# Kernel optimization log

Measured on AMD Instinct MI355X. Metric: run time of the kernel, lower is better.

The kernel has to match this reference:

```python
import jax, jax.numpy as jnp
import numpy as np

# dims
B, S = 1, 32768          # batch, grid seqlen (32^3 latent grid)
NQ, NE = 32768, 262144   # mesh query nodes, grid->query edges
IN, EMB, HID, BOT, PREDH, OUT, NDIM = 192, 192, 192, 192, 192, 4, 3
MAX_WAVELENGTH = 10000.0


def sincos_embed(coords, dim, ndim):
    # ContinuousSincosEmbed: dim % ndim == 0 and (dim//ndim) even here -> no padding
    eff = dim // ndim                                     # 64 dims per coordinate
    omega = 1.0 / MAX_WAVELENGTH ** (jnp.arange(0, eff, 2, dtype=jnp.float32) / eff)  # [eff//2]
    out = coords[..., None] * omega                       # [N, ndim, eff//2]
    emb = jnp.concatenate([jnp.sin(out), jnp.cos(out)], axis=-1)  # [N, ndim, eff]
    return emb.reshape(coords.shape[0], ndim * eff)       # [N, dim]


def _linear_params(key, fan_in, fan_out):
    k1, k2 = jax.random.split(key)
    lim = 1.0 / np.sqrt(fan_in)
    w = jax.random.uniform(k1, (fan_in, fan_out), jnp.float32, -lim, lim)
    b = jax.random.uniform(k2, (fan_out,), jnp.float32, -lim, lim)
    return w, b


def setup_inputs() -> dict:
    key = jax.random.key(0)
    ks = jax.random.split(key, 10)
    x = jax.random.normal(ks[0], (B, S, IN), jnp.float32)
    query_pos = jax.random.uniform(ks[1], (NQ, NDIM), jnp.float32) * 100.0
    # edges sorted by query index (required by the CSR segment reduce in the original)
    qidx = jnp.sort(jax.random.randint(ks[2], (NE,), 0, NQ))
    gidx = jax.random.randint(ks[3], (NE,), 0, B * S)
    grid_to_query_edges = jnp.stack([qidx, gidx], axis=1).astype(jnp.int64)
    proj_w, proj_b = _linear_params(ks[4], IN, EMB)
    msg0_w, msg0_b = _linear_params(ks[5], 2 * EMB, 2 * HID)
    msg1_w, msg1_b = _linear_params(ks[6], 2 * HID, 2 * HID)
    msg2_w, msg2_b = _linear_params(ks[7], 2 * HID, BOT)
    pred0_w, pred0_b = _linear_params(ks[8], BOT, PREDH)
    pred1_w, pred1_b = _linear_params(ks[9], PREDH, OUT)
    return dict(x=x, query_pos=query_pos, grid_to_query_edges=grid_to_query_edges,
                proj_w=proj_w, proj_b=proj_b,
                msg0_w=msg0_w, msg0_b=msg0_b, msg1_w=msg1_w, msg1_b=msg1_b,
                msg2_w=msg2_w, msg2_b=msg2_b,
                pred0_w=pred0_w, pred0_b=pred0_b, pred1_w=pred1_w, pred1_b=pred1_b)


def reference(x, query_pos, grid_to_query_edges,
              proj_w, proj_b, msg0_w, msg0_b, msg1_w, msg1_b, msg2_w, msg2_b,
              pred0_w, pred0_b, pred1_w, pred1_b):
    gelu = lambda t: jax.nn.gelu(t, approximate=False)  # torch nn.GELU default (erf)
    # flatten grid tokens and project
    xf = x.reshape(-1, x.shape[-1]) @ proj_w + proj_b          # [B*S, EMB]
    qe = sincos_embed(query_pos, EMB, NDIM)                    # [NQ, EMB]
    qidx = grid_to_query_edges[:, 0]
    gidx = grid_to_query_edges[:, 1]
    # gather + concat per edge
    h = jnp.concatenate([xf[gidx], qe[qidx]], axis=1)          # [NE, 2*EMB]
    # message MLP
    h = gelu(h @ msg0_w + msg0_b)
    h = gelu(h @ msg1_w + msg1_b)
    h = h @ msg2_w + msg2_b                                    # [NE, BOT]
    # segment mean to query nodes (empty segments -> 0, matching segment_csr mean)
    nq = query_pos.shape[0]
    seg_sum = jax.ops.segment_sum(h, qidx, num_segments=nq)    # [NQ, BOT]
    cnt = jax.ops.segment_sum(jnp.ones((qidx.shape[0], 1), h.dtype), qidx, num_segments=nq)
    m = seg_sum / jnp.maximum(cnt, 1.0)
    # prediction head
    out = gelu(m @ pred0_w + pred0_b) @ pred1_w + pred1_b      # [NQ, OUT]
    return out
```

## Files before the change

kernel.cpp:

```cpp
#include <hip/hip_runtime.h>
#include <math.h>

#define N_Q    32768
#define N_E    262144

typedef _Float16 half8 __attribute__((ext_vector_type(8)));
typedef _Float16 half4v __attribute__((ext_vector_type(4)));
typedef float f32x4 __attribute__((ext_vector_type(4)));

__device__ __forceinline__ float gelu_f(float x) {
    float ax = fabsf(x);
    float t = __builtin_amdgcn_rcpf(fmaf(0.33269070724668f, ax, 1.0f));
    float poly = t * fmaf(t, fmaf(t, 0.7478556f, -0.0958798f), 0.3480242f);
    float e = exp2f(-0.72134752044448f * ax * ax);
    float u = fmaf(-poly, e, 1.0f);
    return 0.5f * fmaf(ax, u, x);
}

__global__ __launch_bounds__(256) void prep_kernel(
    const float* __restrict__ proj_w, const float* __restrict__ proj_b,
    const float* __restrict__ msg0_w, const float* __restrict__ msg0_b,
    float* __restrict__ Wc, float* __restrict__ bc)
{
    int gid = blockIdx.x * 256 + threadIdx.x;
    if (gid < 73728) {
        int j = gid / 384, n = gid - j * 384;
        float a = 0.0f;
        for (int k = 0; k < 192; ++k)
            a = fmaf(proj_w[j * 192 + k], msg0_w[k * 384 + n], a);
        Wc[gid] = a;
    } else if (gid < 73728 + 384) {
        int n = gid - 73728;
        float a = msg0_b[n];
        for (int k = 0; k < 192; ++k)
            a = fmaf(proj_b[k], msg0_w[k * 384 + n], a);
        bc[n] = a;
    }
}

__device__ __forceinline__ void pack_one(const float* __restrict__ W,
                                         _Float16* __restrict__ Wp,
                                         int K, int N, int blk0, int tid) {
    int u = blk0 * 256 + tid;
    if (u * 8 >= K * N) return;
    int l = u & 63, blk = u >> 6;
    int nks = K >> 5;
    int ntile = blk / nks, ks = blk - ntile * nks;
    int n = ntile * 16 + (l & 15);
    int k0 = ks * 32 + (l >> 4) * 8;
    half8 v;
    #pragma unroll
    for (int j = 0; j < 8; ++j) v[j] = (_Float16)W[(size_t)(k0 + j) * N + n];
    *(half8*)(Wp + (size_t)u * 8) = v;
}

__global__ __launch_bounds__(256) void pack_all_kernel(
    const float* __restrict__ Wc,  _Float16* __restrict__ WpC,
    const float* __restrict__ m0,  _Float16* __restrict__ WpQ,
    const float* __restrict__ m1,  _Float16* __restrict__ Wp1,
    const float* __restrict__ m2,  _Float16* __restrict__ Wp2,
    const float* __restrict__ hw,  _Float16* __restrict__ WpH) {
    int b = blockIdx.x, t = threadIdx.x;
    if      (b < 36)  pack_one(Wc,          WpC, 192, 384, b,       t);
    else if (b < 72)  pack_one(m0 + 73728,  WpQ, 192, 384, b - 36,  t);
    else if (b < 144) pack_one(m1,          Wp1, 384, 384, b - 72,  t);
    else if (b < 180) pack_one(m2,          Wp2, 384, 192, b - 144, t);
    else              pack_one(hw,          WpH, 192, 192, b - 180, t);
}

#define PK 200

__global__ __launch_bounds__(256, 2) void pg_kernel(
    const float* __restrict__ x, const _Float16* __restrict__ WpC,
    const float* __restrict__ bc, _Float16* __restrict__ pg)
{
    __shared__ _Float16 hA[64 * PK];
    const int t = threadIdx.x;
    const int r0 = blockIdx.x * 64;
    const int lane = t & 63;
    const int w = t >> 6;
    const int ln = lane & 15, lq = lane >> 4;

    #pragma unroll
    for (int i = 0; i < 12; ++i) {
        int idx = t + 256 * i;
        int r = idx / 48, c4 = idx - r * 48;
        float4 v = ((const float4*)(x + (size_t)(r0 + r) * 192))[c4];
        half4v hv; hv[0] = (_Float16)v.x; hv[1] = (_Float16)v.y;
        hv[2] = (_Float16)v.z; hv[3] = (_Float16)v.w;
        *(half4v*)(hA + r * PK + c4 * 4) = hv;
    }
    __syncthreads();

    f32x4 acc[4][6];
    #pragma unroll
    for (int nt = 0; nt < 6; ++nt) {
        f32x4 bv = *(const f32x4*)(bc + w * 96 + nt * 16 + lq * 4);
        #pragma unroll
        for (int mt = 0; mt < 4; ++mt) acc[mt][nt] = bv;
    }
    #pragma unroll 2
    for (int ks = 0; ks < 6; ++ks) {
        half8 a[4], bf[6];
        #pragma unroll
        for (int mt = 0; mt < 4; ++mt)
            a[mt] = *(const half8*)(hA + (mt * 16 + ln) * PK + ks * 32 + lq * 8);
        #pragma unroll
        for (int nt = 0; nt < 6; ++nt)
            bf[nt] = *(const half8*)(WpC + (size_t)(((w * 6 + nt) * 6 + ks) * 512 + lane * 8));
        #pragma unroll
        for (int nt = 0; nt < 6; ++nt)
            #pragma unroll
            for (int mt = 0; mt < 4; ++mt)
                acc[mt][nt] = __builtin_amdgcn_mfma_f32_16x16x32_f16(bf[nt], a[mt], acc[mt][nt], 0, 0, 0);
    }
    #pragma unroll
    for (int mt = 0; mt < 4; ++mt)
        #pragma unroll
        for (int nt = 0; nt < 6; ++nt) {
            half4v hv;
            #pragma unroll
            for (int r = 0; r < 4; ++r) hv[r] = (_Float16)acc[mt][nt][r];
            *(half4v*)(pg + (size_t)(r0 + mt * 16 + ln) * 384 + w * 96 + nt * 16 + lq * 4) = hv;
        }
}

__global__ __launch_bounds__(256, 2) void pq_kernel(
    const float* __restrict__ qpos, const _Float16* __restrict__ WpQ,
    _Float16* __restrict__ pq)
{
    __shared__ _Float16 hA[64 * PK];
    const int t = threadIdx.x;
    const int r0 = blockIdx.x * 64;
    const int lane = t & 63;
    const int w = t >> 6;
    const int ln = lane & 15, lq = lane >> 4;

    #pragma unroll
    for (int it = 0; it < 24; ++it) {
        int g2 = t + 256 * it;
        int r = g2 / 96, rem = g2 - r * 96;
        int d = rem >> 5, i = rem & 31;
        float omega = exp2f(-(float)i * 0.41524101186092029f);
        float arg = qpos[(size_t)(r0 + r) * 3 + d] * omega;
        float rev = arg * 0.15915494309189535f;
        rev = rev - floorf(rev);
        hA[r * PK + d * 64 + i]      = (_Float16)__builtin_amdgcn_sinf(rev);
        hA[r * PK + d * 64 + 32 + i] = (_Float16)__builtin_amdgcn_cosf(rev);
    }
    __syncthreads();

    f32x4 acc[4][6];
    #pragma unroll
    for (int nt = 0; nt < 6; ++nt)
        #pragma unroll
        for (int mt = 0; mt < 4; ++mt) acc[mt][nt] = (f32x4){0.f, 0.f, 0.f, 0.f};
    #pragma unroll 2
    for (int ks = 0; ks < 6; ++ks) {
        half8 a[4], bf[6];
        #pragma unroll
        for (int mt = 0; mt < 4; ++mt)
            a[mt] = *(const half8*)(hA + (mt * 16 + ln) * PK + ks * 32 + lq * 8);
        #pragma unroll
        for (int nt = 0; nt < 6; ++nt)
            bf[nt] = *(const half8*)(WpQ + (size_t)(((w * 6 + nt) * 6 + ks) * 512 + lane * 8));
        #pragma unroll
        for (int nt = 0; nt < 6; ++nt)
            #pragma unroll
            for (int mt = 0; mt < 4; ++mt)
                acc[mt][nt] = __builtin_amdgcn_mfma_f32_16x16x32_f16(bf[nt], a[mt], acc[mt][nt], 0, 0, 0);
    }
    #pragma unroll
    for (int mt = 0; mt < 4; ++mt)
        #pragma unroll
        for (int nt = 0; nt < 6; ++nt) {
            half4v hv;
            #pragma unroll
            for (int r = 0; r < 4; ++r) hv[r] = (_Float16)acc[mt][nt][r];
            *(half4v*)(pq + (size_t)(r0 + mt * 16 + ln) * 384 + w * 96 + nt * 16 + lq * 4) = hv;
        }
}

#define PADK 392
#define H2S  196

__global__ __launch_bounds__(512, 6) void edge_mlp_kernel(
    const _Float16* __restrict__ pg, const _Float16* __restrict__ pq,
    const int* __restrict__ edges,
    const _Float16* __restrict__ Wp1, const float* __restrict__ b1,
    const _Float16* __restrict__ Wp2, const float* __restrict__ b2,
    float* __restrict__ seg, float* __restrict__ cnt)
{
    __shared__ _Float16 hA[64 * PADK];
    __shared__ int qi[64];
    float* h2 = (float*)hA;

    const int t = threadIdx.x;
    const int e0 = blockIdx.x * 64;
    const int lane = t & 63;
    const int w = t >> 6;
    const int ln = lane & 15;
    const int lq = lane >> 4;

    if (t < 64) qi[t] = edges[2 * (e0 + t)];

    {
        const int m = t >> 3;
        const int cl = t & 7;
        int2 eg = ((const int2*)edges)[e0 + m];
        const half8* gsrc = (const half8*)(pg + (size_t)eg.y * 384) + cl;
        const half8* qsrc = (const half8*)(pq + (size_t)eg.x * 384) + cl;
        half8* dst = (half8*)(hA + m * PADK + cl * 8);
        #pragma unroll
        for (int i = 0; i < 6; ++i) {
            half8 va = gsrc[i * 8];
            half8 vb = qsrc[i * 8];
            half8 o;
            #pragma unroll
            for (int j = 0; j < 8; ++j)
                o[j] = (_Float16)gelu_f((float)va[j] + (float)vb[j]);
            dst[i * 8] = o;
        }
    }
    __syncthreads();

    {
        f32x4 acc[4][3];
        #pragma unroll
        for (int nt = 0; nt < 3; ++nt) {
            f32x4 bv = *(const f32x4*)(b1 + w * 48 + nt * 16 + lq * 4);
            #pragma unroll
            for (int mt = 0; mt < 4; ++mt) acc[mt][nt] = bv;
        }
        #pragma unroll 2
        for (int ks = 0; ks < 12; ++ks) {
            half8 a[4], bf[3];
            #pragma unroll
            for (int mt = 0; mt < 4; ++mt)
                a[mt] = *(const half8*)(hA + (mt * 16 + ln) * PADK + ks * 32 + lq * 8);
            #pragma unroll
            for (int nt = 0; nt < 3; ++nt)
                bf[nt] = *(const half8*)(Wp1 + (size_t)(((w * 3 + nt) * 12 + ks) * 512 + lane * 8));
            #pragma unroll
            for (int nt = 0; nt < 3; ++nt)
                #pragma unroll
                for (int mt = 0; mt < 4; ++mt)
                    acc[mt][nt] = __builtin_amdgcn_mfma_f32_16x16x32_f16(bf[nt], a[mt], acc[mt][nt], 0, 0, 0);
        }
        __syncthreads();
        #pragma unroll
        for (int mt = 0; mt < 4; ++mt)
            #pragma unroll
            for (int nt = 0; nt < 3; ++nt) {
                half4v hv;
                #pragma unroll
                for (int r = 0; r < 4; ++r) hv[r] = (_Float16)gelu_f(acc[mt][nt][r]);
                *(half4v*)(hA + (mt * 16 + ln) * PADK + w * 48 + nt * 16 + lq * 4) = hv;
            }
        __syncthreads();
    }

    {
        const int n0 = (w & 3) * 48;
        const int mh = (w >> 2) * 2;
        f32x4 acc[2][3];
        #pragma unroll
        for (int nt = 0; nt < 3; ++nt) {
            f32x4 bv = *(const f32x4*)(b2 + n0 + nt * 16 + lq * 4);
            #pragma unroll
            for (int mt = 0; mt < 2; ++mt) acc[mt][nt] = bv;
        }
        #pragma unroll 2
        for (int ks = 0; ks < 12; ++ks) {
            half8 a[2], bf[3];
            #pragma unroll
            for (int mt = 0; mt < 2; ++mt)
                a[mt] = *(const half8*)(hA + ((mh + mt) * 16 + ln) * PADK + ks * 32 + lq * 8);
            #pragma unroll
            for (int nt = 0; nt < 3; ++nt)
                bf[nt] = *(const half8*)(Wp2 + (size_t)((((w & 3) * 3 + nt) * 12 + ks) * 512 + lane * 8));
            #pragma unroll
            for (int nt = 0; nt < 3; ++nt)
                #pragma unroll
                for (int mt = 0; mt < 2; ++mt)
                    acc[mt][nt] = __builtin_amdgcn_mfma_f32_16x16x32_f16(bf[nt], a[mt], acc[mt][nt], 0, 0, 0);
        }
        __syncthreads();
        #pragma unroll
        for (int mt = 0; mt < 2; ++mt)
            #pragma unroll
            for (int nt = 0; nt < 3; ++nt)
                *(f32x4*)(h2 + ((mh + mt) * 16 + ln) * H2S + n0 + nt * 16 + lq * 4) = acc[mt][nt];
        __syncthreads();
    }

    if (t < 384) {
        int half_ = t >= 192;
        int col = t - half_ * 192;
        int mlo = half_ * 32, mhi = mlo + 32;
        float a = 0.0f;
        for (int m = mlo; m < mhi; ++m) {
            a += h2[m * H2S + col];
            if (m == mhi - 1 || qi[m + 1] != qi[m]) {
                atomicAdd(&seg[(size_t)qi[m] * 192 + col], a);
                a = 0.0f;
            }
        }
    } else if (t < 386) {
        int half_ = t - 384;
        int mlo = half_ * 32, mhi = mlo + 32;
        float run = 1.0f;
        for (int m = mlo + 1; m < mhi; ++m) {
            if (qi[m] != qi[m - 1]) { atomicAdd(&cnt[qi[m - 1]], run); run = 1.0f; }
            else run += 1.0f;
        }
        atomicAdd(&cnt[qi[mhi - 1]], run);
    }
}

#define PSK 196

__global__ __launch_bounds__(256, 2) void head_kernel(
    const float* __restrict__ seg, const float* __restrict__ cnt,
    const _Float16* __restrict__ Wp0, const float* __restrict__ b0,
    const float* __restrict__ w1, const float* __restrict__ b1,
    float* __restrict__ out)
{
    __shared__ _Float16 hA[64 * PK];
    __shared__ float ps[64 * PSK];
    __shared__ float w1s[192 * 4];
    __shared__ float invc[64];
    const int t = threadIdx.x;
    const int r0 = blockIdx.x * 64;
    const int lane = t & 63;
    const int w = t >> 6;
    const int ln = lane & 15, lq = lane >> 4;

    if (t < 64) invc[t] = 1.0f / fmaxf(cnt[r0 + t], 1.0f);
    if (t < 192) ((float4*)w1s)[t] = ((const float4*)w1)[t];
    __syncthreads();

    #pragma unroll
    for (int i = 0; i < 12; ++i) {
        int idx = t + 256 * i;
        int r = idx / 48, c4 = idx - r * 48;
        float inv = invc[r];
        float4 v = ((const float4*)(seg + (size_t)(r0 + r) * 192))[c4];
        half4v hv; hv[0] = (_Float16)(v.x * inv); hv[1] = (_Float16)(v.y * inv);
        hv[2] = (_Float16)(v.z * inv); hv[3] = (_Float16)(v.w * inv);
        *(half4v*)(hA + r * PK + c4 * 4) = hv;
    }
    __syncthreads();

    f32x4 acc[4][3];
    #pragma unroll
    for (int nt = 0; nt < 3; ++nt) {
        f32x4 bv = *(const f32x4*)(b0 + w * 48 + nt * 16 + lq * 4);
        #pragma unroll
        for (int mt = 0; mt < 4; ++mt) acc[mt][nt] = bv;
    }
    #pragma unroll 2
    for (int ks = 0; ks < 6; ++ks) {
        half8 a[4], bf[3];
        #pragma unroll
        for (int mt = 0; mt < 4; ++mt)
            a[mt] = *(const half8*)(hA + (mt * 16 + ln) * PK + ks * 32 + lq * 8);
        #pragma unroll
        for (int nt = 0; nt < 3; ++nt)
            bf[nt] = *(const half8*)(Wp0 + (size_t)(((w * 3 + nt) * 6 + ks) * 512 + lane * 8));
        #pragma unroll
        for (int nt = 0; nt < 3; ++nt)
            #pragma unroll
            for (int mt = 0; mt < 4; ++mt)
                acc[mt][nt] = __builtin_amdgcn_mfma_f32_16x16x32_f16(bf[nt], a[mt], acc[mt][nt], 0, 0, 0);
    }
    #pragma unroll
    for (int mt = 0; mt < 4; ++mt)
        #pragma unroll
        for (int nt = 0; nt < 3; ++nt) {
            f32x4 g;
            #pragma unroll
            for (int r = 0; r < 4; ++r) g[r] = gelu_f(acc[mt][nt][r]);
            *(f32x4*)(ps + (mt * 16 + ln) * PSK + w * 48 + nt * 16 + lq * 4) = g;
        }
    __syncthreads();

    {
        int r = t >> 2, oo = t & 3;
        float a = b1[oo];
        for (int k = 0; k < 192; ++k)
            a = fmaf(ps[r * PSK + k], w1s[k * 4 + oo], a);
        out[(size_t)(r0 + r) * 4 + oo] = a;
    }
}

extern "C" void kernel_launch(void* const* d_in, const int* in_sizes, int n_in,
                              void* d_out, int out_size, void* d_ws, size_t ws_size,
                              hipStream_t stream) {
    (void)in_sizes; (void)n_in; (void)out_size; (void)ws_size;
    const float* x       = (const float*)d_in[0];
    const float* qpos    = (const float*)d_in[1];
    const int*   edges   = (const int*)d_in[2];
    const float* proj_w  = (const float*)d_in[3];
    const float* proj_b  = (const float*)d_in[4];
    const float* msg0_w  = (const float*)d_in[5];
    const float* msg0_b  = (const float*)d_in[6];
    const float* msg1_w  = (const float*)d_in[7];
    const float* msg1_b  = (const float*)d_in[8];
    const float* msg2_w  = (const float*)d_in[9];
    const float* msg2_b  = (const float*)d_in[10];
    const float* pred0_w = (const float*)d_in[11];
    const float* pred0_b = (const float*)d_in[12];
    const float* pred1_w = (const float*)d_in[13];
    const float* pred1_b = (const float*)d_in[14];
    float* out = (float*)d_out;

    char* ws = (char*)d_ws;
    _Float16* pg  = (_Float16*)(ws);
    _Float16* pq  = (_Float16*)(ws + 25165824);
    float*    seg = (float*)(ws + 50331648);
    float*    cnt = (float*)(ws + 75497472);
    float*    Wc  = (float*)(ws + 75628544);
    float*    bc  = (float*)(ws + 75923456);
    _Float16* WpC = (_Float16*)(ws + 75924992);
    _Float16* WpQ = (_Float16*)(ws + 76072448);
    _Float16* Wp1 = (_Float16*)(ws + 76219904);
    _Float16* Wp2 = (_Float16*)(ws + 76514816);
    _Float16* WpH = (_Float16*)(ws + 76662272);

    hipMemsetAsync(seg, 0, 25165824 + 131072, stream);
    prep_kernel<<<290, 256, 0, stream>>>(proj_w, proj_b, msg0_w, msg0_b, Wc, bc);
    pack_all_kernel<<<198, 256, 0, stream>>>(Wc, WpC, msg0_w, WpQ,
                                             msg1_w, Wp1, msg2_w, Wp2,
                                             pred0_w, WpH);
    pg_kernel<<<512, 256, 0, stream>>>(x, WpC, bc, pg);
    pq_kernel<<<512, 256, 0, stream>>>(qpos, WpQ, pq);
    edge_mlp_kernel<<<4096, 512, 0, stream>>>(pg, pq, edges,
                                              Wp1, msg1_b, Wp2, msg2_b,
                                              seg, cnt);
    head_kernel<<<512, 256, 0, stream>>>(seg, cnt, WpH, pred0_b,
                                         pred1_w, pred1_b, out);
}
```

Before: 345.9 us.

## Fuse prep/pack and pg/pq kernels, halve row tiles, vectorize segment atomics

Merges the weight-combine and packing kernels into one launch that writes the combined proj·msg0 weight directly in packed fp16 layout, removing the fp32 intermediate. The pg and pq projection kernels are merged into a single launch with 32-row tiles, doubling the grid. The head kernel also moves to 32-row tiles with more blocks per CU. In the edge kernel's segment reduction, each thread now handles two columns with float2 loads. The aim is fewer launches and better occupancy, at the cost of less weight reuse per block and some idle threads.

```diff
diff --git a/kernel.cpp b/kernel.cpp
--- a/kernel.cpp
+++ b/kernel.cpp
@@ -15,27 +15,6 @@
     float e = exp2f(-0.72134752044448f * ax * ax);
     float u = fmaf(-poly, e, 1.0f);
     return 0.5f * fmaf(ax, u, x);
-}
-
-__global__ __launch_bounds__(256) void prep_kernel(
-    const float* __restrict__ proj_w, const float* __restrict__ proj_b,
-    const float* __restrict__ msg0_w, const float* __restrict__ msg0_b,
-    float* __restrict__ Wc, float* __restrict__ bc)
-{
-    int gid = blockIdx.x * 256 + threadIdx.x;
-    if (gid < 73728) {
-        int j = gid / 384, n = gid - j * 384;
-        float a = 0.0f;
-        for (int k = 0; k < 192; ++k)
-            a = fmaf(proj_w[j * 192 + k], msg0_w[k * 384 + n], a);
-        Wc[gid] = a;
-    } else if (gid < 73728 + 384) {
-        int n = gid - 73728;
-        float a = msg0_b[n];
-        for (int k = 0; k < 192; ++k)
-            a = fmaf(proj_b[k], msg0_w[k * 384 + n], a);
-        bc[n] = a;
-    }
 }
 
 __device__ __forceinline__ void pack_one(const float* __restrict__ W,
@@ -54,130 +33,118 @@
     *(half8*)(Wp + (size_t)u * 8) = v;
 }
 
-__global__ __launch_bounds__(256) void pack_all_kernel(
-    const float* __restrict__ Wc,  _Float16* __restrict__ WpC,
-    const float* __restrict__ m0,  _Float16* __restrict__ WpQ,
-    const float* __restrict__ m1,  _Float16* __restrict__ Wp1,
-    const float* __restrict__ m2,  _Float16* __restrict__ Wp2,
-    const float* __restrict__ hw,  _Float16* __restrict__ WpH) {
+__global__ __launch_bounds__(256, 4) void preppack_kernel(
+    const float* __restrict__ proj_w, const float* __restrict__ proj_b,
+    const float* __restrict__ msg0_w, const float* __restrict__ msg0_b,
+    const float* __restrict__ msg1_w, const float* __restrict__ msg2_w,
+    const float* __restrict__ pred0_w,
+    _Float16* __restrict__ WpC, float* __restrict__ bc,
+    _Float16* __restrict__ WpQ, _Float16* __restrict__ Wp1,
+    _Float16* __restrict__ Wp2, _Float16* __restrict__ WpH)
+{
     int b = blockIdx.x, t = threadIdx.x;
-    if      (b < 36)  pack_one(Wc,          WpC, 192, 384, b,       t);
-    else if (b < 72)  pack_one(m0 + 73728,  WpQ, 192, 384, b - 36,  t);
-    else if (b < 144) pack_one(m1,          Wp1, 384, 384, b - 72,  t);
-    else if (b < 180) pack_one(m2,          Wp2, 384, 192, b - 144, t);
-    else              pack_one(hw,          WpH, 192, 192, b - 180, t);
+    if (b < 290) {
+        int gid = b * 256 + t;
+        if (gid < 73728) {
+            int j = gid / 384, n = gid - j * 384;
+            float a = 0.0f;
+            for (int k = 0; k < 192; ++k)
+                a = fmaf(proj_w[j * 192 + k], msg0_w[k * 384 + n], a);
+            int off = (((n >> 4) * 6 + (j >> 5)) * 512) +
+                      ((((j >> 3) & 3) * 16 + (n & 15)) * 8) + (j & 7);
+            WpC[off] = (_Float16)a;
+        } else if (gid < 73728 + 384) {
+            int n = gid - 73728;
+            float a = msg0_b[n];
+            for (int k = 0; k < 192; ++k)
+                a = fmaf(proj_b[k], msg0_w[k * 384 + n], a);
+            bc[n] = a;
+        }
+    } else {
+        int p = b - 290;
+        if      (p < 36)  pack_one(msg0_w + 73728, WpQ, 192, 384, p,       t);
+        else if (p < 108) pack_one(msg1_w,         Wp1, 384, 384, p - 36,  t);
+        else if (p < 144) pack_one(msg2_w,         Wp2, 384, 192, p - 108, t);
+        else              pack_one(pred0_w,        WpH, 192, 192, p - 144, t);
+    }
 }
 
 #define PK 200
 
-__global__ __launch_bounds__(256, 2) void pg_kernel(
-    const float* __restrict__ x, const _Float16* __restrict__ WpC,
-    const float* __restrict__ bc, _Float16* __restrict__ pg)
+__global__ __launch_bounds__(256, 4) void pgpq_kernel(
+    const float* __restrict__ x, const float* __restrict__ qpos,
+    const _Float16* __restrict__ WpC, const _Float16* __restrict__ WpQ,
+    const float* __restrict__ bc,
+    _Float16* __restrict__ pg, _Float16* __restrict__ pq)
 {
-    __shared__ _Float16 hA[64 * PK];
+    __shared__ _Float16 hA[32 * PK];
     const int t = threadIdx.x;
-    const int r0 = blockIdx.x * 64;
+    const bool isPg = blockIdx.x < 1024;
+    const int r0 = (isPg ? blockIdx.x : blockIdx.x - 1024) * 32;
     const int lane = t & 63;
     const int w = t >> 6;
     const int ln = lane & 15, lq = lane >> 4;
 
-    #pragma unroll
-    for (int i = 0; i < 12; ++i) {
-        int idx = t + 256 * i;
-        int r = idx / 48, c4 = idx - r * 48;
-        float4 v = ((const float4*)(x + (size_t)(r0 + r) * 192))[c4];
-        half4v hv; hv[0] = (_Float16)v.x; hv[1] = (_Float16)v.y;
-        hv[2] = (_Float16)v.z; hv[3] = (_Float16)v.w;
-        *(half4v*)(hA + r * PK + c4 * 4) = hv;
+    if (isPg) {
+        #pragma unroll
+        for (int i = 0; i < 6; ++i) {
+            int idx = t + 256 * i;
+            int r = idx / 48, c4 = idx - r * 48;
+            float4 v = ((const float4*)(x + (size_t)(r0 + r) * 192))[c4];
+            half4v hv; hv[0] = (_Float16)v.x; hv[1] = (_Float16)v.y;
+            hv[2] = (_Float16)v.z; hv[3] = (_Float16)v.w;
+            *(half4v*)(hA + r * PK + c4 * 4) = hv;
+        }
+    } else {
+        #pragma unroll
+        for (int it = 0; it < 12; ++it) {
+            int g2 = t + 256 * it;
+            int r = g2 / 96, rem = g2 - r * 96;
+            int d = rem >> 5, i = rem & 31;
+            float omega = exp2f(-(float)i * 0.41524101186092029f);
+            float arg = qpos[(size_t)(r0 + r) * 3 + d] * omega;
+            float rev = arg * 0.15915494309189535f;
+            rev = rev - floorf(rev);
+            hA[r * PK + d * 64 + i]      = (_Float16)__builtin_amdgcn_sinf(rev);
+            hA[r * PK + d * 64 + 32 + i] = (_Float16)__builtin_amdgcn_cosf(rev);
+        }
     }
     __syncthreads();
 
-    f32x4 acc[4][6];
+    const _Float16* __restrict__ Wp = isPg ? WpC : WpQ;
+    _Float16* __restrict__ out = isPg ? pg : pq;
+
+    f32x4 acc[2][6];
     #pragma unroll
     for (int nt = 0; nt < 6; ++nt) {
-        f32x4 bv = *(const f32x4*)(bc + w * 96 + nt * 16 + lq * 4);
-        #pragma unroll
-        for (int mt = 0; mt < 4; ++mt) acc[mt][nt] = bv;
+        f32x4 bv = isPg ? *(const f32x4*)(bc + w * 96 + nt * 16 + lq * 4)
+                        : (f32x4){0.f, 0.f, 0.f, 0.f};
+        #pragma unroll
+        for (int mt = 0; mt < 2; ++mt) acc[mt][nt] = bv;
     }
     #pragma unroll 2
     for (int ks = 0; ks < 6; ++ks) {
-        half8 a[4], bf[6];
-        #pragma unroll
-        for (int mt = 0; mt < 4; ++mt)
+        half8 a[2], bf[6];
+        #pragma unroll
+        for (int mt = 0; mt < 2; ++mt)
             a[mt] = *(const half8*)(hA + (mt * 16 + ln) * PK + ks * 32 + lq * 8);
         #pragma unroll
         for (int nt = 0; nt < 6; ++nt)
-            bf[nt] = *(const half8*)(WpC + (size_t)(((w * 6 + nt) * 6 + ks) * 512 + lane * 8));
+            bf[nt] = *(const half8*)(Wp + (size_t)(((w * 6 + nt) * 6 + ks) * 512 + lane * 8));
         #pragma unroll
         for (int nt = 0; nt < 6; ++nt)
             #pragma unroll
-            for (int mt = 0; mt < 4; ++mt)
+            for (int mt = 0; mt < 2; ++mt)
                 acc[mt][nt] = __builtin_amdgcn_mfma_f32_16x16x32_f16(bf[nt], a[mt], acc[mt][nt], 0, 0, 0);
     }
     #pragma unroll
-    for (int mt = 0; mt < 4; ++mt)
+    for (int mt = 0; mt < 2; ++mt)
         #pragma unroll
         for (int nt = 0; nt < 6; ++nt) {
             half4v hv;
             #pragma unroll
             for (int r = 0; r < 4; ++r) hv[r] = (_Float16)acc[mt][nt][r];
-            *(half4v*)(pg + (size_t)(r0 + mt * 16 + ln) * 384 + w * 96 + nt * 16 + lq * 4) = hv;
-        }
-}
-
-__global__ __launch_bounds__(256, 2) void pq_kernel(
-    const float* __restrict__ qpos, const _Float16* __restrict__ WpQ,
-    _Float16* __restrict__ pq)
-{
-    __shared__ _Float16 hA[64 * PK];
-    const int t = threadIdx.x;
-    const int r0 = blockIdx.x * 64;
-    const int lane = t & 63;
-    const int w = t >> 6;
-    const int ln = lane & 15, lq = lane >> 4;
-
-    #pragma unroll
-    for (int it = 0; it < 24; ++it) {
-        int g2 = t + 256 * it;
-        int r = g2 / 96, rem = g2 - r * 96;
-        int d = rem >> 5, i = rem & 31;
-        float omega = exp2f(-(float)i * 0.41524101186092029f);
-        float arg = qpos[(size_t)(r0 + r) * 3 + d] * omega;
-        float rev = arg * 0.15915494309189535f;
-        rev = rev - floorf(rev);
-        hA[r * PK + d * 64 + i]      = (_Float16)__builtin_amdgcn_sinf(rev);
-        hA[r * PK + d * 64 + 32 + i] = (_Float16)__builtin_amdgcn_cosf(rev);
-    }
-    __syncthreads();
-
-    f32x4 acc[4][6];
-    #pragma unroll
-    for (int nt = 0; nt < 6; ++nt)
-        #pragma unroll
-        for (int mt = 0; mt < 4; ++mt) acc[mt][nt] = (f32x4){0.f, 0.f, 0.f, 0.f};
-    #pragma unroll 2
-    for (int ks = 0; ks < 6; ++ks) {
-        half8 a[4], bf[6];
-        #pragma unroll
-        for (int mt = 0; mt < 4; ++mt)
-            a[mt] = *(const half8*)(hA + (mt * 16 + ln) * PK + ks * 32 + lq * 8);
-        #pragma unroll
-        for (int nt = 0; nt < 6; ++nt)
-            bf[nt] = *(const half8*)(WpQ + (size_t)(((w * 6 + nt) * 6 + ks) * 512 + lane * 8));
-        #pragma unroll
-        for (int nt = 0; nt < 6; ++nt)
-            #pragma unroll
-            for (int mt = 0; mt < 4; ++mt)
-                acc[mt][nt] = __builtin_amdgcn_mfma_f32_16x16x32_f16(bf[nt], a[mt], acc[mt][nt], 0, 0, 0);
-    }
-    #pragma unroll
-    for (int mt = 0; mt < 4; ++mt)
-        #pragma unroll
-        for (int nt = 0; nt < 6; ++nt) {
-            half4v hv;
-            #pragma unroll
-            for (int r = 0; r < 4; ++r) hv[r] = (_Float16)acc[mt][nt][r];
-            *(half4v*)(pq + (size_t)(r0 + mt * 16 + ln) * 384 + w * 96 + nt * 16 + lq * 4) = hv;
+            *(half4v*)(out + (size_t)(r0 + mt * 16 + ln) * 384 + w * 96 + nt * 16 + lq * 4) = hv;
         }
 }
 
@@ -294,19 +261,22 @@
         __syncthreads();
     }
 
-    if (t < 384) {
-        int half_ = t >= 192;
-        int col = t - half_ * 192;
+    if (t < 192) {
+        int half_ = t / 96;
+        int cp = t - half_ * 96;
+        int col = cp * 2;
         int mlo = half_ * 32, mhi = mlo + 32;
-        float a = 0.0f;
+        float ax = 0.0f, ay = 0.0f;
         for (int m = mlo; m < mhi; ++m) {
-            a += h2[m * H2S + col];
+            float2 v = *(const float2*)(h2 + m * H2S + col);
+            ax += v.x; ay += v.y;
             if (m == mhi - 1 || qi[m + 1] != qi[m]) {
-                atomicAdd(&seg[(size_t)qi[m] * 192 + col], a);
-                a = 0.0f;
+                atomicAdd(&seg[(size_t)qi[m] * 192 + col], ax);
+                atomicAdd(&seg[(size_t)qi[m] * 192 + col + 1], ay);
+                ax = 0.0f; ay = 0.0f;
             }
         }
-    } else if (t < 386) {
+    } else if (t >= 384 && t < 386) {
         int half_ = t - 384;
         int mlo = half_ * 32, mhi = mlo + 32;
         float run = 1.0f;
@@ -320,28 +290,28 @@
 
 #define PSK 196
 
-__global__ __launch_bounds__(256, 2) void head_kernel(
+__global__ __launch_bounds__(256, 3) void head_kernel(
     const float* __restrict__ seg, const float* __restrict__ cnt,
     const _Float16* __restrict__ Wp0, const float* __restrict__ b0,
     const float* __restrict__ w1, const float* __restrict__ b1,
     float* __restrict__ out)
 {
-    __shared__ _Float16 hA[64 * PK];
-    __shared__ float ps[64 * PSK];
+    __shared__ _Float16 hA[32 * PK];
+    __shared__ float ps[32 * PSK];
     __shared__ float w1s[192 * 4];
-    __shared__ float invc[64];
+    __shared__ float invc[32];
     const int t = threadIdx.x;
-    const int r0 = blockIdx.x * 64;
+    const int r0 = blockIdx.x * 32;
     const int lane = t & 63;
     const int w = t >> 6;
     const int ln = lane & 15, lq = lane >> 4;
 
-    if (t < 64) invc[t] = 1.0f / fmaxf(cnt[r0 + t], 1.0f);
+    if (t < 32) invc[t] = 1.0f / fmaxf(cnt[r0 + t], 1.0f);
     if (t < 192) ((float4*)w1s)[t] = ((const float4*)w1)[t];
     __syncthreads();
 
     #pragma unroll
-    for (int i = 0; i < 12; ++i) {
+    for (int i = 0; i < 6; ++i) {
         int idx = t + 256 * i;
         int r = idx / 48, c4 = idx - r * 48;
         float inv = invc[r];
@@ -352,18 +322,18 @@
     }
     __syncthreads();
 
-    f32x4 acc[4][3];
+    f32x4 acc[2][3];
     #pragma unroll
     for (int nt = 0; nt < 3; ++nt) {
         f32x4 bv = *(const f32x4*)(b0 + w * 48 + nt * 16 + lq * 4);
         #pragma unroll
-        for (int mt = 0; mt < 4; ++mt) acc[mt][nt] = bv;
+        for (int mt = 0; mt < 2; ++mt) acc[mt][nt] = bv;
     }
     #pragma unroll 2
     for (int ks = 0; ks < 6; ++ks) {
-        half8 a[4], bf[3];
-        #pragma unroll
-        for (int mt = 0; mt < 4; ++mt)
+        half8 a[2], bf[3];
+        #pragma unroll
+        for (int mt = 0; mt < 2; ++mt)
             a[mt] = *(const half8*)(hA + (mt * 16 + ln) * PK + ks * 32 + lq * 8);
         #pragma unroll
         for (int nt = 0; nt < 3; ++nt)
@@ -371,11 +341,11 @@
         #pragma unroll
         for (int nt = 0; nt < 3; ++nt)
             #pragma unroll
-            for (int mt = 0; mt < 4; ++mt)
+            for (int mt = 0; mt < 2; ++mt)
                 acc[mt][nt] = __builtin_amdgcn_mfma_f32_16x16x32_f16(bf[nt], a[mt], acc[mt][nt], 0, 0, 0);
     }
     #pragma unroll
-    for (int mt = 0; mt < 4; ++mt)
+    for (int mt = 0; mt < 2; ++mt)
         #pragma unroll
         for (int nt = 0; nt < 3; ++nt) {
             f32x4 g;
@@ -385,7 +355,7 @@
         }
     __syncthreads();
 
-    {
+    if (t < 128) {
         int r = t >> 2, oo = t & 3;
         float a = b1[oo];
         for (int k = 0; k < 192; ++k)
@@ -420,24 +390,21 @@
     _Float16* pq  = (_Float16*)(ws + 25165824);
     float*    seg = (float*)(ws + 50331648);
     float*    cnt = (float*)(ws + 75497472);
-    float*    Wc  = (float*)(ws + 75628544);
-    float*    bc  = (float*)(ws + 75923456);
-    _Float16* WpC = (_Float16*)(ws + 75924992);
-    _Float16* WpQ = (_Float16*)(ws + 76072448);
-    _Float16* Wp1 = (_Float16*)(ws + 76219904);
-    _Float16* Wp2 = (_Float16*)(ws + 76514816);
-    _Float16* WpH = (_Float16*)(ws + 76662272);
+    float*    bc  = (float*)(ws + 75628544);
+    _Float16* WpC = (_Float16*)(ws + 75630080);
+    _Float16* WpQ = (_Float16*)(ws + 75777536);
+    _Float16* Wp1 = (_Float16*)(ws + 75924992);
+    _Float16* Wp2 = (_Float16*)(ws + 76219904);
+    _Float16* WpH = (_Float16*)(ws + 76367360);
 
     hipMemsetAsync(seg, 0, 25165824 + 131072, stream);
-    prep_kernel<<<290, 256, 0, stream>>>(proj_w, proj_b, msg0_w, msg0_b, Wc, bc);
-    pack_all_kernel<<<198, 256, 0, stream>>>(Wc, WpC, msg0_w, WpQ,
-                                             msg1_w, Wp1, msg2_w, Wp2,
-                                             pred0_w, WpH);
-    pg_kernel<<<512, 256, 0, stream>>>(x, WpC, bc, pg);
-    pq_kernel<<<512, 256, 0, stream>>>(qpos, WpQ, pq);
+    preppack_kernel<<<452, 256, 0, stream>>>(proj_w, proj_b, msg0_w, msg0_b,
+                                             msg1_w, msg2_w, pred0_w,
+                                             WpC, bc, WpQ, Wp1, Wp2, WpH);
+    pgpq_kernel<<<2048, 256, 0, stream>>>(x, qpos, WpC, WpQ, bc, pg, pq);
     edge_mlp_kernel<<<4096, 512, 0, stream>>>(pg, pq, edges,
                                               Wp1, msg1_b, Wp2, msg2_b,
                                               seg, cnt);
-    head_kernel<<<512, 256, 0, stream>>>(seg, cnt, WpH, pred0_b,
-                                         pred1_w, pred1_b, out);
-}
+    head_kernel<<<1024, 256, 0, stream>>>(seg, cnt, WpH, pred0_b,
+                                          pred1_w, pred1_b, out);
+}
```

New measurement: 351.1 us. Within noise of the previous version (+1.5%).
